# Optimization experiments

Hardware: AMD Instinct MI355X
Metric: run time of the kernel (lower is better)

## Reference

```python
import jax, jax.numpy as jnp
import numpy as np

DT = 0.001
HIDDEN = 512
OUT = 128

def setup_inputs() -> dict:
    key = jax.random.key(0)
    k1, k2 = jax.random.split(key)
    x = jax.random.normal(k1, (64, 2048, HIDDEN), dtype=jnp.float32)
    # torch Linear default init ~ U(-1/sqrt(fan_in), 1/sqrt(fan_in)), weight shape [out, in]
    lim = 1.0 / np.sqrt(HIDDEN)
    W = jax.random.uniform(k2, (OUT, HIDDEN), dtype=jnp.float32, minval=-lim, maxval=lim)
    tau_syn = jnp.asarray(0.5, dtype=jnp.float32)  # tau_syn_out (used as tau_syn_inv)
    tau_mem = jnp.asarray(0.5, dtype=jnp.float32)  # tau_mem_out (used as tau_mem_inv)
    return {"x": x, "W": W, "tau_syn": tau_syn, "tau_mem": tau_mem}

def reference(x, W, tau_syn, tau_mem):
    # SNNDecode.forward: clamp taus, permute to [seq, batch, in], per-step
    # Linear + norse LI (leaky integrator) feed-forward step with v_leak = 0.
    tau_syn = jnp.clip(tau_syn, 0.0, 1.0)
    tau_mem = jnp.clip(tau_mem, 0.0, 1.0)
    batch, seq, _ = x.shape
    # The per-step Linear is recurrence-independent: hoist it into one big GEMM.
    # z_all: [seq, batch, out]
    z_all = jnp.einsum('bsh,oh->sbo', x, W)
    v0 = jnp.zeros((batch, OUT), dtype=x.dtype)
    i0 = jnp.zeros((batch, OUT), dtype=x.dtype)

    def step(carry, z):
        v, i = carry
        # li_feed_forward_step: dv = dt*tau_mem_inv*((v_leak - v) + i)
        v_new = v + DT * tau_mem * (i - v)
        i_dec = i - DT * tau_syn * i
        i_new = i_dec + z
        return (v_new, i_new), v_new

    (v_f, i_f), voltages = jax.lax.scan(step, (v0, i0), z_all)
    # output stacked over time: [seq, batch, out]; final state (v, i)
    return voltages, v_f, i_f
```

## Files before the change

### kernel.cpp

```cpp
#include <hip/hip_runtime.h>
#include <hip/hip_bf16.h>


typedef __attribute__((ext_vector_type(4))) float          f4;
typedef __attribute__((ext_vector_type(8))) short          s8;
typedef __attribute__((ext_vector_type(4))) unsigned       u4;
typedef __attribute__((ext_vector_type(2))) unsigned       u2;
typedef __attribute__((ext_vector_type(4))) unsigned short su4;

#define SEQ    2048
#define HID    512
#define CHAINS 8192
#define VOLT   16777216
#define NCH    64
#define CHUNK  32

__device__ __forceinline__ float clamp01(float x) { return fminf(fmaxf(x, 0.f), 1.f); }

__device__ __forceinline__ unsigned pkbf(float x, float y) {
  float2 t; t.x = x; t.y = y;
  union { __hip_bfloat162 h; unsigned u; } c;
  c.h = __float22bfloat162_rn(t);
  return c.u;
}

__device__ __forceinline__ short f2bf(float f) {
  union { float f; unsigned u; } c; c.f = f;
  unsigned u = c.u;
  unsigned r = (u + 0x7fffu + ((u >> 16) & 1u)) >> 16;
  return (short)r;
}

__device__ __forceinline__ float bf2f(unsigned short s) {
  union { unsigned u; float f; } c; c.u = ((unsigned)s) << 16; return c.f;
}

__device__ __forceinline__ int swz(int row, int k) {
  return (row * 64 + k) ^ ((row & 7) << 3);
}

__global__ __launch_bounds__(256) void k_wconv(const float* __restrict__ W,
                                               unsigned short* __restrict__ Wb) {
  const int i = blockIdx.x * 256 + threadIdx.x;
  const f4 lo = ((const f4*)W)[2 * i];
  const f4 hi = ((const f4*)W)[2 * i + 1];
  s8 v;
#pragma unroll
  for (int j = 0; j < 4; ++j) { v[j] = f2bf(lo[j]); v[j + 4] = f2bf(hi[j]); }
  ((s8*)Wb)[i] = v;
}

template <int ZB>
__global__ __launch_bounds__(256, 2) void k_gemm(const float* __restrict__ X,
                                                 const unsigned short* __restrict__ Wb,
                                                 float* __restrict__ Out,
                                                 unsigned short* __restrict__ zbf,
                                                 const float* __restrict__ tau_syn,
                                                 const float* __restrict__ tau_mem,
                                                 float* __restrict__ ws) {
  __shared__ __align__(16) char smem[65536];
  short* const AS = (short*)smem;
  float* const ZS = (float*)smem;

  const int tid = threadIdx.x;
  const int blk = blockIdx.x;
  const int m0  = blk << 7;
  const int bI  = blk >> 4;
  const int t0  = (blk & 15) << 7;

  const int rbase = tid >> 3;
  const int coff  = (tid & 7) << 3;

  const int lane = tid & 63;
  const int wid  = tid >> 6;
  const int wmb  = (wid >> 1) << 6;
  const int wnb  = (wid & 1) << 6;
  const int lr   = lane & 15;
  const int lk   = (lane >> 4) << 3;

  const float* pX[4];
#pragma unroll
  for (int c = 0; c < 4; ++c)
    pX[c] = X + (size_t)(m0 + (c << 5) + rbase) * HID + coff;
  const unsigned short* pB[4];
#pragma unroll
  for (int ni = 0; ni < 4; ++ni)
    pB[ni] = Wb + (size_t)(wnb + (ni << 4) + lr) * HID + lk;

  f4 acc[4][4];
#pragma unroll
  for (int mi = 0; mi < 4; ++mi)
#pragma unroll
    for (int ni = 0; ni < 4; ++ni) acc[mi][ni] = (f4){0.f, 0.f, 0.f, 0.f};

  f4 xa[3][4][2];
#pragma unroll
  for (int c = 0; c < 4; ++c) {
    xa[0][c][0] = *(const f4*)(pX[c]);
    xa[0][c][1] = *(const f4*)(pX[c] + 4);
    xa[1][c][0] = *(const f4*)(pX[c] + 64);
    xa[1][c][1] = *(const f4*)(pX[c] + 68);
  }

#pragma unroll
  for (int ks = 0; ks < 8; ++ks) {
    const int cur = ks % 3;
    short* const Ac = AS + ((ks & 1) << 13);
#pragma unroll
    for (int c = 0; c < 4; ++c) {
      const int row = (c << 5) + rbase;
      u4 va;
      va[0] = pkbf(xa[cur][c][0][0], xa[cur][c][0][1]);
      va[1] = pkbf(xa[cur][c][0][2], xa[cur][c][0][3]);
      va[2] = pkbf(xa[cur][c][1][0], xa[cur][c][1][1]);
      va[3] = pkbf(xa[cur][c][1][2], xa[cur][c][1][3]);
      *(u4*)&Ac[swz(row, coff)] = va;
    }
    __syncthreads();
    s8 bg[2][4];
#pragma unroll
    for (int kk = 0; kk < 2; ++kk)
#pragma unroll
      for (int ni = 0; ni < 4; ++ni)
        bg[kk][ni] = *(const s8*)(pB[ni] + (ks << 6) + (kk << 5));
    if (ks < 6) {
      const int k0 = (ks + 2) << 6;
      const int nxt = (ks + 2) % 3;
#pragma unroll
      for (int c = 0; c < 4; ++c) {
        xa[nxt][c][0] = *(const f4*)(pX[c] + k0);
        xa[nxt][c][1] = *(const f4*)(pX[c] + k0 + 4);
      }
    }
#pragma unroll
    for (int kk = 0; kk < 2; ++kk) {
      s8 af[4];
#pragma unroll
      for (int mi = 0; mi < 4; ++mi)
        af[mi] = *(const s8*)&Ac[swz(wmb + (mi << 4) + lr, (kk << 5) + lk)];
#pragma unroll
      for (int mi = 0; mi < 4; ++mi)
#pragma unroll
        for (int ni = 0; ni < 4; ++ni)
          acc[mi][ni] = __builtin_amdgcn_mfma_f32_16x16x32_bf16(af[mi], bg[kk][ni],
                                                                acc[mi][ni], 0, 0, 0);
    }
  }

  __syncthreads();
  const int rr = (lane >> 4) << 2;
#pragma unroll
  for (int mi = 0; mi < 4; ++mi)
#pragma unroll
    for (int ni = 0; ni < 4; ++ni)
#pragma unroll
      for (int r = 0; r < 4; ++r)
        ZS[(wmb + (mi << 4) + rr + r) * 128 + wnb + (ni << 4) + lr] = acc[mi][ni][r];
  __syncthreads();

  if (ZB) {
    unsigned short* const Zrow = zbf + (size_t)t0 * 8192 + (bI << 7);
#pragma unroll
    for (int i = 0; i < 16; ++i) {
      const int idx  = (i << 8) + tid;
      const int toff = idx >> 5;
      const int c4   = idx & 31;
      const f4 zv = *(const f4*)&ZS[toff * 128 + (c4 << 2)];
      u2 pk; pk[0] = pkbf(zv[0], zv[1]); pk[1] = pkbf(zv[2], zv[3]);
      *(u2*)(Zrow + (size_t)toff * 8192 + (c4 << 2)) = pk;
    }
  } else {
    float* const Zrow = Out + (size_t)t0 * 8192 + (bI << 7);
#pragma unroll
    for (int i = 0; i < 16; ++i) {
      const int idx  = (i << 8) + tid;
      const int toff = idx >> 5;
      const int c4   = idx & 31;
      *(f4*)(Zrow + (size_t)toff * 8192 + (c4 << 2)) = *(const f4*)&ZS[toff * 128 + (c4 << 2)];
    }
  }
  {
    const float a  = 0.001f * clamp01(tau_mem[0]);
    const float eb = 1.f - 0.001f * clamp01(tau_syn[0]);
    const int col = tid & 127, h = tid >> 7;
    const int chain = (bI << 7) + col;
#pragma unroll
    for (int s = 0; s < 2; ++s) {
      const int r0 = (h << 6) + (s << 5);
      const float* zs = ZS + r0 * 128 + col;
      float v = 0.f, ii = 0.f;
#pragma unroll 8
      for (int j = 0; j < CHUNK; ++j) {
        const float z = zs[j * 128];
        v  = v + a * (ii - v);
        ii = eb * ii + z;
      }
      const int q = ((blk & 15) << 2) + (h << 1) + s;
      ws[q * CHAINS + chain]                 = v;
      ws[NCH * CHAINS + q * CHAINS + chain]  = ii;
    }
  }
}

template <int ZB>
__global__ __launch_bounds__(256) void k_emit(const float* __restrict__ tau_syn,
                                              const float* __restrict__ tau_mem,
                                              float* __restrict__ Out,
                                              const unsigned short* __restrict__ zbf,
                                              const float* __restrict__ ws) {
  const int tid = threadIdx.x;
  const int cg = (blockIdx.x & 31) * 64 + (tid & 63);
  const int q  = (blockIdx.x >> 5) * 4 + (tid >> 6);
  const float a  = 0.001f * clamp01(tau_mem[0]);
  const float bb = 0.001f * clamp01(tau_syn[0]);
  const float ea = 1.f - a, eb = 1.f - bb;
  float P = 1.f, Q = 0.f, R = 1.f;
#pragma unroll
  for (int j = 0; j < CHUNK; ++j) { float Pn = P * ea; Q = P * a + Q * eb; P = Pn; R *= eb; }

  const f4* vend = (const f4*)ws;
  const f4* iend = vend + NCH * 2048;
  f4 sv = (f4){0.f, 0.f, 0.f, 0.f}, si = (f4){0.f, 0.f, 0.f, 0.f};
#pragma unroll 4
  for (int p = 0; p < q; ++p) {
    const f4 ve = vend[p * 2048 + cg];
    const f4 ie = iend[p * 2048 + cg];
    const f4 nv = P * sv + Q * si + ve;
    si = R * si + ie;
    sv = nv;
  }

  f4* o4 = (f4*)Out;
  const int tb = q << 5;
  f4 v = sv, ii = si;
#pragma unroll 8
  for (int j = 0; j < CHUNK; ++j) {
    const size_t idx = (size_t)(tb + j) * 2048 + cg;
    f4 z;
    if (ZB) {
      const su4 zb = *(const su4*)(zbf + (((size_t)(tb + j)) << 13) + (cg << 2));
      z[0] = bf2f(zb[0]); z[1] = bf2f(zb[1]); z[2] = bf2f(zb[2]); z[3] = bf2f(zb[3]);
    } else {
      z = o4[idx];
    }
    v  = v + a * (ii - v);
    o4[idx] = v;
    ii = eb * ii + z;
  }
  if (q == NCH - 1) {
    ((f4*)(Out + VOLT))[cg]          = v;
    ((f4*)(Out + VOLT + CHAINS))[cg] = ii;
  }
}

extern "C" void kernel_launch(void* const* d_in, const int* in_sizes, int n_in,
                              void* d_out, int out_size, void* d_ws, size_t ws_size,
                              hipStream_t stream) {
  const float* X   = (const float*)d_in[0];
  const float* W   = (const float*)d_in[1];
  const float* tsy = (const float*)d_in[2];
  const float* tme = (const float*)d_in[3];
  float* Out = (float*)d_out;
  float* ws  = (float*)d_ws;
  unsigned short* Wb  = (unsigned short*)((char*)d_ws + (4u << 20));
  unsigned short* zbf = (unsigned short*)((char*)d_ws + (4u << 20) + (128u << 10));
  const size_t need = (4ull << 20) + (128ull << 10) + (32ull << 20);

  k_wconv<<<32, 256, 0, stream>>>(W, Wb);
  if (ws_size >= need) {
    k_gemm<1><<<1024, 256, 0, stream>>>(X, Wb, Out, zbf, tsy, tme, ws);
    k_emit<1><<<512, 256, 0, stream>>>(tsy, tme, Out, zbf, ws);
  } else {
    k_gemm<0><<<1024, 256, 0, stream>>>(X, Wb, Out, zbf, tsy, tme, ws);
    k_emit<0><<<512, 256, 0, stream>>>(tsy, tme, Out, zbf, ws);
  }
}
```

Measured before the change: 104.3 us.

## Stage GEMM output tile as swizzled bf16 in LDS to raise occupancy

The GEMM epilogue now writes the accumulator tile to shared memory as bf16 instead of fp32, with an XOR swizzle on the column index. This halves the shared allocation to 32 KB and raises the launch-bounds occupancy hint from 2 to 4 blocks per CU, aiming to hide global-memory latency on the large X stream. The swizzle is meant to avoid LDS bank conflicts on both the row-wise store pass and the column-wise chunk-scan reads. In exchange, the fp32 output path and the per-chunk scan now consume bf16-rounded z values, so accuracy drops, and the higher occupancy target may squeeze register allocation.

```diff
diff --git a/kernel.cpp b/kernel.cpp
--- a/kernel.cpp
+++ b/kernel.cpp
@@ -5,7 +5,6 @@
 typedef __attribute__((ext_vector_type(4))) float          f4;
 typedef __attribute__((ext_vector_type(8))) short          s8;
 typedef __attribute__((ext_vector_type(4))) unsigned       u4;
-typedef __attribute__((ext_vector_type(2))) unsigned       u2;
 typedef __attribute__((ext_vector_type(4))) unsigned short su4;
 
 #define SEQ    2048
@@ -24,11 +23,11 @@
   return c.u;
 }
 
-__device__ __forceinline__ short f2bf(float f) {
+__device__ __forceinline__ unsigned short f2bf(float f) {
   union { float f; unsigned u; } c; c.f = f;
   unsigned u = c.u;
   unsigned r = (u + 0x7fffu + ((u >> 16) & 1u)) >> 16;
-  return (short)r;
+  return (unsigned short)r;
 }
 
 __device__ __forceinline__ float bf2f(unsigned short s) {
@@ -37,6 +36,10 @@
 
 __device__ __forceinline__ int swz(int row, int k) {
   return (row * 64 + k) ^ ((row & 7) << 3);
+}
+
+__device__ __forceinline__ int zidx(int row, int col) {
+  return row * 128 + (col ^ (((row >> 2) & 7) << 4));
 }
 
 __global__ __launch_bounds__(256) void k_wconv(const float* __restrict__ W,
@@ -44,23 +47,24 @@
   const int i = blockIdx.x * 256 + threadIdx.x;
   const f4 lo = ((const f4*)W)[2 * i];
   const f4 hi = ((const f4*)W)[2 * i + 1];
-  s8 v;
-#pragma unroll
-  for (int j = 0; j < 4; ++j) { v[j] = f2bf(lo[j]); v[j + 4] = f2bf(hi[j]); }
-  ((s8*)Wb)[i] = v;
+  su4 v0, v1;
+#pragma unroll
+  for (int j = 0; j < 4; ++j) { v0[j] = f2bf(lo[j]); v1[j] = f2bf(hi[j]); }
+  ((su4*)Wb)[2 * i] = v0;
+  ((su4*)Wb)[2 * i + 1] = v1;
 }
 
 template <int ZB>
-__global__ __launch_bounds__(256, 2) void k_gemm(const float* __restrict__ X,
+__global__ __launch_bounds__(256, 4) void k_gemm(const float* __restrict__ X,
                                                  const unsigned short* __restrict__ Wb,
                                                  float* __restrict__ Out,
                                                  unsigned short* __restrict__ zbf,
                                                  const float* __restrict__ tau_syn,
                                                  const float* __restrict__ tau_mem,
                                                  float* __restrict__ ws) {
-  __shared__ __align__(16) char smem[65536];
-  short* const AS = (short*)smem;
-  float* const ZS = (float*)smem;
+  __shared__ __align__(16) char smem[32768];
+  short* const AS           = (short*)smem;
+  unsigned short* const ZSb = (unsigned short*)smem;
 
   const int tid = threadIdx.x;
   const int blk = blockIdx.x;
@@ -155,28 +159,23 @@
     for (int ni = 0; ni < 4; ++ni)
 #pragma unroll
       for (int r = 0; r < 4; ++r)
-        ZS[(wmb + (mi << 4) + rr + r) * 128 + wnb + (ni << 4) + lr] = acc[mi][ni][r];
+        ZSb[zidx(wmb + (mi << 4) + rr + r, wnb + (ni << 4) + lr)] =
+            f2bf(acc[mi][ni][r]);
   __syncthreads();
 
-  if (ZB) {
-    unsigned short* const Zrow = zbf + (size_t)t0 * 8192 + (bI << 7);
-#pragma unroll
-    for (int i = 0; i < 16; ++i) {
-      const int idx  = (i << 8) + tid;
-      const int toff = idx >> 5;
-      const int c4   = idx & 31;
-      const f4 zv = *(const f4*)&ZS[toff * 128 + (c4 << 2)];
-      u2 pk; pk[0] = pkbf(zv[0], zv[1]); pk[1] = pkbf(zv[2], zv[3]);
-      *(u2*)(Zrow + (size_t)toff * 8192 + (c4 << 2)) = pk;
-    }
-  } else {
-    float* const Zrow = Out + (size_t)t0 * 8192 + (bI << 7);
-#pragma unroll
-    for (int i = 0; i < 16; ++i) {
-      const int idx  = (i << 8) + tid;
-      const int toff = idx >> 5;
-      const int c4   = idx & 31;
-      *(f4*)(Zrow + (size_t)toff * 8192 + (c4 << 2)) = *(const f4*)&ZS[toff * 128 + (c4 << 2)];
+#pragma unroll
+  for (int i = 0; i < 16; ++i) {
+    const int idx  = (i << 8) + tid;
+    const int toff = idx >> 5;
+    const int c4   = idx & 31;
+    const int colp = (c4 << 2) ^ (((toff >> 2) & 7) << 4);
+    const su4 zb = *(const su4*)&ZSb[toff * 128 + colp];
+    if (ZB) {
+      *(su4*)(zbf + (size_t)(t0 + toff) * 8192 + (bI << 7) + (c4 << 2)) = zb;
+    } else {
+      f4 zf; zf[0] = bf2f(zb[0]); zf[1] = bf2f(zb[1]);
+      zf[2] = bf2f(zb[2]); zf[3] = bf2f(zb[3]);
+      *(f4*)(Out + (size_t)(t0 + toff) * 8192 + (bI << 7) + (c4 << 2)) = zf;
     }
   }
   {
@@ -187,11 +186,10 @@
 #pragma unroll
     for (int s = 0; s < 2; ++s) {
       const int r0 = (h << 6) + (s << 5);
-      const float* zs = ZS + r0 * 128 + col;
       float v = 0.f, ii = 0.f;
 #pragma unroll 8
       for (int j = 0; j < CHUNK; ++j) {
-        const float z = zs[j * 128];
+        const float z = bf2f(ZSb[zidx(r0 + j, col)]);
         v  = v + a * (ii - v);
         ii = eb * ii + z;
       }
```

New measurement: 180.2 us. +72.7%, slower.

## Replace serial chunk-carry prefix in emit with parallel scan kernel

Applied to the files above, without the earlier changes.

Adds a separate kernel that runs a Hillis-Steele parallel prefix scan in shared memory over the 64 per-chunk end states. It replaces the serial O(q) loop in which every emit thread re-read all earlier chunk states from global memory. The emit kernel then just loads its precomputed carry-in state. This costs an extra kernel launch and a round trip of the carry states through the workspace. The weight conversion store is also split into two 8-byte stores.

```diff
diff --git a/kernel.cpp b/kernel.cpp
--- a/kernel.cpp
+++ b/kernel.cpp
@@ -24,11 +24,11 @@
   return c.u;
 }
 
-__device__ __forceinline__ short f2bf(float f) {
+__device__ __forceinline__ unsigned short f2bf(float f) {
   union { float f; unsigned u; } c; c.f = f;
   unsigned u = c.u;
   unsigned r = (u + 0x7fffu + ((u >> 16) & 1u)) >> 16;
-  return (short)r;
+  return (unsigned short)r;
 }
 
 __device__ __forceinline__ float bf2f(unsigned short s) {
@@ -44,10 +44,11 @@
   const int i = blockIdx.x * 256 + threadIdx.x;
   const f4 lo = ((const f4*)W)[2 * i];
   const f4 hi = ((const f4*)W)[2 * i + 1];
-  s8 v;
-#pragma unroll
-  for (int j = 0; j < 4; ++j) { v[j] = f2bf(lo[j]); v[j + 4] = f2bf(hi[j]); }
-  ((s8*)Wb)[i] = v;
+  su4 v0, v1;
+#pragma unroll
+  for (int j = 0; j < 4; ++j) { v0[j] = f2bf(lo[j]); v1[j] = f2bf(hi[j]); }
+  ((su4*)Wb)[2 * i] = v0;
+  ((su4*)Wb)[2 * i + 1] = v1;
 }
 
 template <int ZB>
@@ -202,6 +203,57 @@
   }
 }
 
+__global__ __launch_bounds__(256) void k_comb(const float* __restrict__ tau_syn,
+                                              const float* __restrict__ tau_mem,
+                                              float* __restrict__ Out,
+                                              float* __restrict__ ws) {
+  __shared__ __align__(16) f4 SV[NCH][4], SI[NCH][4];
+  const int tid = threadIdx.x;
+  const int q   = tid >> 2;
+  const int s   = tid & 3;
+  const int cg  = blockIdx.x * 4 + s;
+  const float a  = 0.001f * clamp01(tau_mem[0]);
+  const float bb = 0.001f * clamp01(tau_syn[0]);
+  const float ea = 1.f - a, eb = 1.f - bb;
+  float P = 1.f, Q = 0.f, R = 1.f;
+#pragma unroll
+  for (int j = 0; j < CHUNK; ++j) { const float Pn = P * ea; Q = P * a + Q * eb; P = Pn; R *= eb; }
+
+  f4* vend = (f4*)ws;
+  f4* iend = vend + NCH * 2048;
+  f4 xv = vend[q * 2048 + cg];
+  f4 xi = iend[q * 2048 + cg];
+  SV[q][s] = xv; SI[q][s] = xi;
+
+  float Pd = P, Qd = Q, Rd = R;
+#pragma unroll
+  for (int d = 1; d < NCH; d <<= 1) {
+    __syncthreads();
+    f4 av, ai;
+    const bool val = (q >= d);
+    if (val) { av = SV[q - d][s]; ai = SI[q - d][s]; }
+    __syncthreads();
+    if (val) {
+      xv = xv + Pd * av + Qd * ai;
+      xi = xi + Rd * ai;
+      SV[q][s] = xv; SI[q][s] = xi;
+    }
+    const float Pn = Pd * Pd;
+    Qd = Pd * Qd + Qd * Rd;
+    Pd = Pn;
+    Rd = Rd * Rd;
+  }
+  __syncthreads();
+  f4 iv = (f4){0.f, 0.f, 0.f, 0.f}, ij = (f4){0.f, 0.f, 0.f, 0.f};
+  if (q > 0) { iv = SV[q - 1][s]; ij = SI[q - 1][s]; }
+  vend[q * 2048 + cg] = iv;
+  iend[q * 2048 + cg] = ij;
+  if (q == NCH - 1) {
+    ((f4*)(Out + VOLT))[cg]          = xv;
+    ((f4*)(Out + VOLT + CHAINS))[cg] = xi;
+  }
+}
+
 template <int ZB>
 __global__ __launch_bounds__(256) void k_emit(const float* __restrict__ tau_syn,
                                               const float* __restrict__ tau_mem,
@@ -212,27 +264,15 @@
   const int cg = (blockIdx.x & 31) * 64 + (tid & 63);
   const int q  = (blockIdx.x >> 5) * 4 + (tid >> 6);
   const float a  = 0.001f * clamp01(tau_mem[0]);
-  const float bb = 0.001f * clamp01(tau_syn[0]);
-  const float ea = 1.f - a, eb = 1.f - bb;
-  float P = 1.f, Q = 0.f, R = 1.f;
-#pragma unroll
-  for (int j = 0; j < CHUNK; ++j) { float Pn = P * ea; Q = P * a + Q * eb; P = Pn; R *= eb; }
-
-  const f4* vend = (const f4*)ws;
-  const f4* iend = vend + NCH * 2048;
-  f4 sv = (f4){0.f, 0.f, 0.f, 0.f}, si = (f4){0.f, 0.f, 0.f, 0.f};
-#pragma unroll 4
-  for (int p = 0; p < q; ++p) {
-    const f4 ve = vend[p * 2048 + cg];
-    const f4 ie = iend[p * 2048 + cg];
-    const f4 nv = P * sv + Q * si + ve;
-    si = R * si + ie;
-    sv = nv;
-  }
+  const float eb = 1.f - 0.001f * clamp01(tau_syn[0]);
+
+  const f4* vin = (const f4*)ws;
+  const f4* iin = vin + NCH * 2048;
+  f4 v  = vin[q * 2048 + cg];
+  f4 ii = iin[q * 2048 + cg];
 
   f4* o4 = (f4*)Out;
   const int tb = q << 5;
-  f4 v = sv, ii = si;
 #pragma unroll 8
   for (int j = 0; j < CHUNK; ++j) {
     const size_t idx = (size_t)(tb + j) * 2048 + cg;
@@ -246,10 +286,6 @@
     v  = v + a * (ii - v);
     o4[idx] = v;
     ii = eb * ii + z;
-  }
-  if (q == NCH - 1) {
-    ((f4*)(Out + VOLT))[cg]          = v;
-    ((f4*)(Out + VOLT + CHAINS))[cg] = ii;
   }
 }
 
@@ -269,9 +305,11 @@
   k_wconv<<<32, 256, 0, stream>>>(W, Wb);
   if (ws_size >= need) {
     k_gemm<1><<<1024, 256, 0, stream>>>(X, Wb, Out, zbf, tsy, tme, ws);
+    k_comb<<<512, 256, 0, stream>>>(tsy, tme, Out, ws);
     k_emit<1><<<512, 256, 0, stream>>>(tsy, tme, Out, zbf, ws);
   } else {
     k_gemm<0><<<1024, 256, 0, stream>>>(X, Wb, Out, zbf, tsy, tme, ws);
+    k_comb<<<512, 256, 0, stream>>>(tsy, tme, Out, ws);
     k_emit<0><<<512, 256, 0, stream>>>(tsy, tme, Out, zbf, ws);
   }
 }
```

Result: no change. 105.0 us (+0.7%).
